# Kernel tuning notes

Hardware: AMD Instinct MI355X
Metric: run time of the kernel (lower is better)

The kernel has to match this reference:

```python
import jax, jax.numpy as jnp
import numpy as np

B, S, H = 4, 2048, 2048          # batch, seq_len, hidden_size
NH, NKV, D = 8, 1, 256           # query heads, kv heads (MQA), head_dim
ROPE_THETA = 10000.0
SCALE = D ** -0.5


def setup_inputs() -> dict:
    key = jax.random.key(0)
    k1, k2, k3 = jax.random.split(key, 3)
    hidden_states = jax.random.normal(k1, (B, S, H), dtype=jnp.float32)
    w_qkv = jax.random.normal(k2, (H, (NH + 2 * NKV) * D), dtype=jnp.float32) * 0.02
    w_o = jax.random.normal(k3, (NH * D, H), dtype=jnp.float32) * 0.02
    positions = jnp.arange(S, dtype=jnp.int32)
    return {"hidden_states": hidden_states, "positions": positions,
            "w_qkv": w_qkv, "w_o": w_o}


def _apply_rope(x, positions):
    # x: [B, S, n_heads, D], neox style: rotate halves
    d2 = D // 2
    inv_freq = 1.0 / (ROPE_THETA ** (jnp.arange(0, d2, dtype=jnp.float32) * 2.0 / D))
    ang = positions.astype(jnp.float32)[:, None] * inv_freq[None, :]      # [S, d2]
    cos = jnp.cos(ang)[None, :, None, :]                                  # [1,S,1,d2]
    sin = jnp.sin(ang)[None, :, None, :]
    x1, x2 = x[..., :d2], x[..., d2:]
    return jnp.concatenate([x1 * cos - x2 * sin, x2 * cos + x1 * sin], axis=-1)


def reference(hidden_states, positions, w_qkv, w_o):
    # fused QKV projection
    qkv = jnp.einsum('bsh,hd->bsd', hidden_states, w_qkv)                 # [B,S,(NH+2NKV)*D]
    q_size, kv_size = NH * D, NKV * D
    q = qkv[..., :q_size].reshape(B, S, NH, D)
    k = qkv[..., q_size:q_size + kv_size].reshape(B, S, NKV, D)
    v = qkv[..., q_size + kv_size:].reshape(B, S, NKV, D)

    q = _apply_rope(q, positions)
    k = _apply_rope(k, positions)

    # expand KV heads for MQA/GQA
    rep = NH // NKV
    k = jnp.repeat(k, rep, axis=2)                                        # [B,S,NH,D]
    v = jnp.repeat(v, rep, axis=2)

    scores = jnp.einsum('bqhd,bkhd->bhqk', q, k) * SCALE                  # [B,NH,S,S]
    causal = jnp.tril(jnp.ones((S, S), dtype=bool))
    scores = jnp.where(causal[None, None], scores, jnp.finfo(scores.dtype).min)
    probs = jax.nn.softmax(scores, axis=-1)
    attn = jnp.einsum('bhqk,bkhd->bqhd', probs, v).reshape(B, S, NH * D)

    return jnp.einsum('bsd,dh->bsh', attn, w_o)                           # [B,S,H]
```

## Files before the change

kernel.cpp:

```cpp
#include <hip/hip_runtime.h>
#include <math.h>

constexpr int BATCH = 4;
constexpr int SEQ   = 2048;
constexpr int HID   = 2048;
constexpr int NHEAD = 8;
constexpr int HD    = 256;
constexpr int QKVN  = (NHEAD + 2) * HD;
constexpr float SCL = 0.0625f;

typedef __bf16 bf16_t;
typedef __bf16 bf16x8 __attribute__((ext_vector_type(8)));
typedef float  f32x4  __attribute__((ext_vector_type(4)));

__device__ __forceinline__ f32x4 zero4() {
  f32x4 z; z[0] = 0.f; z[1] = 0.f; z[2] = 0.f; z[3] = 0.f; return z;
}

__device__ __forceinline__ f32x4 mfma16(bf16x8 a, bf16x8 b, f32x4 c) {
  return __builtin_amdgcn_mfma_f32_16x16x32_bf16(a, b, c, 0, 0, 0);
}

__device__ __forceinline__ void gl2lds16(const void* g, void* lds) {
  typedef __attribute__((address_space(1))) void* gp_t;
  typedef __attribute__((address_space(3))) void* lp_t;
  __builtin_amdgcn_global_load_lds((gp_t)(size_t)g,
                                   (lp_t)(unsigned int)(size_t)lds, 16, 0, 0);
}

__device__ __forceinline__ float rmax16(float v) {
#pragma unroll
  for (int o = 1; o < 16; o <<= 1) v = fmaxf(v, __shfl_xor(v, o));
  return v;
}
__device__ __forceinline__ float rsum16(float v) {
#pragma unroll
  for (int o = 1; o < 16; o <<= 1) v += __shfl_xor(v, o);
  return v;
}

__global__ __launch_bounds__(256)
void cvt_bf16_kernel(const float* __restrict__ in, bf16_t* __restrict__ out) {
  const int i = blockIdx.x * 256 + threadIdx.x;
  const float4 a = ((const float4*)in)[i * 2];
  const float4 b = ((const float4*)in)[i * 2 + 1];
  bf16x8 o;
  o[0] = (bf16_t)a.x; o[1] = (bf16_t)a.y; o[2] = (bf16_t)a.z; o[3] = (bf16_t)a.w;
  o[4] = (bf16_t)b.x; o[5] = (bf16_t)b.y; o[6] = (bf16_t)b.z; o[7] = (bf16_t)b.w;
  ((bf16x8*)out)[i] = o;
}

__global__ __launch_bounds__(256)
void transw_kernel(const float* __restrict__ w, bf16_t* __restrict__ wT, int K, int N) {
  __shared__ __align__(16) bf16_t tile[64][72];
  const int n0 = blockIdx.x * 64, k0 = blockIdx.y * 64;
  const int t = threadIdx.x, rr = t >> 3, c8 = (t & 7) * 8;
#pragma unroll
  for (int it = 0; it < 2; ++it) {
    const int r = rr + it * 32;
    const float4* p = (const float4*)(w + (size_t)(k0 + r) * N + n0 + c8);
    const float4 a = p[0], b = p[1];
    bf16x8 o;
    o[0] = (bf16_t)a.x; o[1] = (bf16_t)a.y; o[2] = (bf16_t)a.z; o[3] = (bf16_t)a.w;
    o[4] = (bf16_t)b.x; o[5] = (bf16_t)b.y; o[6] = (bf16_t)b.z; o[7] = (bf16_t)b.w;
    *(bf16x8*)&tile[r][c8] = o;
  }
  __syncthreads();
#pragma unroll
  for (int it = 0; it < 2; ++it) {
    const int rn = rr + it * 32;
    bf16x8 o;
#pragma unroll
    for (int j = 0; j < 8; ++j) o[j] = tile[c8 + j][rn];
    *(bf16x8*)&wT[(size_t)(n0 + rn) * K + k0 + c8] = o;
  }
}

#define BAR()   __builtin_amdgcn_s_barrier()
#define LGKM0() do { asm volatile("s_waitcnt lgkmcnt(0)" ::: "memory"); \
                     __builtin_amdgcn_sched_barrier(0); } while (0)
#define VMC(n)  asm volatile("s_waitcnt vmcnt(" #n ")" ::: "memory")

template <typename TC>
__global__ __launch_bounds__(512)
void gemm256_kernel(const bf16_t* __restrict__ A, const bf16_t* __restrict__ BT,
                    TC* __restrict__ C, int M, int N, int K) {
  __shared__ __align__(16) bf16_t As[2][2][128 * 64];
  __shared__ __align__(16) bf16_t Bs[2][2][128 * 64];

  const int tid = threadIdx.x;
  const int w = tid >> 6, lane = tid & 63;
  const int wr = w >> 2, wc = w & 3;
  const int quad = lane >> 4, l15 = lane & 15;
  const int bm = blockIdx.y * 256, bn = blockIdx.x * 256;

  const int srow = tid >> 3;
  const int sc16 = (tid & 7) ^ (srow & 7);
  const bf16_t* Asrc = A  + (size_t)(bm + srow) * K + sc16 * 8;
  const bf16_t* Bsrc = BT + (size_t)(bn + srow) * K + sc16 * 8;

#define STAGE_A(t, h) do {                                                  \
    const bf16_t* _s = Asrc + (size_t)((h) * 128) * K + (t) * 64;           \
    gl2lds16(_s,                 &As[(t) & 1][h][w * 512]);                 \
    gl2lds16(_s + (size_t)64 * K, &As[(t) & 1][h][4096 + w * 512]);         \
  } while (0)
#define STAGE_B(t, h) do {                                                  \
    const bf16_t* _s = Bsrc + (size_t)((h) * 128) * K + (t) * 64;           \
    gl2lds16(_s,                 &Bs[(t) & 1][h][w * 512]);                 \
    gl2lds16(_s + (size_t)64 * K, &Bs[(t) & 1][h][4096 + w * 512]);         \
  } while (0)

  const int c0  = ((quad ^ (l15 & 7)) << 3);
  const int aro = l15 * 64;
  const int bh  = wc >> 1;
  const int bro = ((wc & 1) * 64 + l15) * 64;

  f32x4 acc[8][4];
#pragma unroll
  for (int mt = 0; mt < 8; ++mt)
#pragma unroll
    for (int nt = 0; nt < 4; ++nt) acc[mt][nt] = zero4();

  bf16x8 bfr[4][2], a01[2][2], a2[6][2];

#define LD_B(b) do { _Pragma("unroll")                                      \
    for (int nt = 0; nt < 4; ++nt) {                                        \
      bfr[nt][0] = *(const bf16x8*)&Bs[b][bh][bro + nt * 1024 + c0];        \
      bfr[nt][1] = *(const bf16x8*)&Bs[b][bh][bro + nt * 1024 + (c0 ^ 32)]; \
    } } while (0)
#define LD_A01(b) do { _Pragma("unroll")                                    \
    for (int mt = 0; mt < 2; ++mt) {                                        \
      a01[mt][0] = *(const bf16x8*)&As[b][wr][aro + mt * 1024 + c0];        \
      a01[mt][1] = *(const bf16x8*)&As[b][wr][aro + mt * 1024 + (c0 ^ 32)]; \
    } } while (0)
#define LD_A2(b) do { _Pragma("unroll")                                     \
    for (int i = 0; i < 6; ++i) {                                           \
      a2[i][0] = *(const bf16x8*)&As[b][wr][aro + (i + 2) * 1024 + c0];     \
      a2[i][1] = *(const bf16x8*)&As[b][wr][aro + (i + 2) * 1024 + (c0^32)];\
    } } while (0)
#define MFMA8(A0, A1, mb) do {                                              \
    __builtin_amdgcn_s_setprio(1);                                          \
    _Pragma("unroll")                                                       \
    for (int nt = 0; nt < 4; ++nt) {                                        \
      acc[(mb)][nt]     = mfma16((A0)[0], bfr[nt][0], acc[(mb)][nt]);       \
      acc[(mb)][nt]     = mfma16((A0)[1], bfr[nt][1], acc[(mb)][nt]);       \
      acc[(mb)+1][nt]   = mfma16((A1)[0], bfr[nt][0], acc[(mb)+1][nt]);     \
      acc[(mb)+1][nt]   = mfma16((A1)[1], bfr[nt][1], acc[(mb)+1][nt]);     \
    }                                                                       \
    __builtin_amdgcn_s_setprio(0);                                          \
  } while (0)

  const int NITER = K >> 7;

  STAGE_A(0, 0); STAGE_A(0, 1); STAGE_B(0, 0); STAGE_B(0, 1);
  STAGE_A(1, 0); STAGE_A(1, 1);
  VMC(4);
  BAR();

  for (int u = 0; u < NITER; ++u) {
    const bool last = (u == NITER - 1);
    const int t1 = 2 * u + 1, t2 = 2 * u + 2, t3 = 2 * u + 3;

    LD_B(0); LD_A01(0);
    STAGE_B(t1, 0);
    BAR(); LGKM0();
    MFMA8(a01[0], a01[1], 0);
    BAR();
    LD_A2(0);
    STAGE_B(t1, 1);
    BAR(); LGKM0();
    MFMA8(a2[0], a2[1], 2);
    BAR();
    if (!last) STAGE_A(t2, 0);
    BAR();
    MFMA8(a2[2], a2[3], 4);
    BAR();
    if (!last) { STAGE_A(t2, 1); VMC(4); } else { VMC(0); }
    BAR();
    MFMA8(a2[4], a2[5], 6);
    BAR();
    LD_B(1); LD_A01(1);
    if (!last) STAGE_B(t2, 0);
    BAR(); LGKM0();
    MFMA8(a01[0], a01[1], 0);
    BAR();
    LD_A2(1);
    if (!last) STAGE_B(t2, 1);
    BAR(); LGKM0();
    MFMA8(a2[0], a2[1], 2);
    BAR();
    if (!last) STAGE_A(t3, 0);
    BAR();
    MFMA8(a2[2], a2[3], 4);
    BAR();
    if (!last) { STAGE_A(t3, 1); VMC(4); }
    BAR();
    MFMA8(a2[4], a2[5], 6);
    BAR();
  }

#pragma unroll
  for (int mt = 0; mt < 8; ++mt)
#pragma unroll
    for (int nt = 0; nt < 4; ++nt)
#pragma unroll
      for (int r = 0; r < 4; ++r) {
        const int row = bm + wr * 128 + mt * 16 + quad * 4 + r;
        const int col = bn + wc * 64 + nt * 16 + l15;
        C[(size_t)row * N + col] = (TC)acc[mt][nt][r];
      }
#undef STAGE_A
#undef STAGE_B
#undef LD_B
#undef LD_A01
#undef LD_A2
#undef MFMA8
}

__global__ __launch_bounds__(128)
void rope_table_kernel(const int* __restrict__ pos, float2* __restrict__ tab) {
  const int s = blockIdx.x, i = threadIdx.x;
  const float inv_freq = powf(10000.0f, -(float)i / 128.0f);
  const float ang = (float)pos[s] * inv_freq;
  float sn, cs;
  sincosf(ang, &sn, &cs);
  tab[s * 128 + i] = make_float2(cs, sn);
}

__global__ __launch_bounds__(256)
void rope_kernel(const float2* __restrict__ tab, bf16_t* __restrict__ qkv) {
  const int bs = blockIdx.x * 16 + (threadIdx.x >> 4);
  const int h  = blockIdx.y;
  const int i0 = (threadIdx.x & 15) * 8;
  const int s  = bs & (SEQ - 1);
  const size_t base = (size_t)bs * QKVN + (size_t)h * HD;
  bf16x8 a = *(const bf16x8*)&qkv[base + i0];
  bf16x8 b = *(const bf16x8*)&qkv[base + 128 + i0];
  bf16x8 oa, ob;
#pragma unroll
  for (int j = 0; j < 8; ++j) {
    const float2 t = tab[s * 128 + i0 + j];
    const float x1 = (float)a[j], x2 = (float)b[j];
    oa[j] = (bf16_t)(x1 * t.x - x2 * t.y);
    ob[j] = (bf16_t)(x2 * t.x + x1 * t.y);
  }
  *(bf16x8*)&qkv[base + i0]       = oa;
  *(bf16x8*)&qkv[base + 128 + i0] = ob;
}

__global__ __launch_bounds__(256)
void vtrans_kernel(const bf16_t* __restrict__ qkv, bf16_t* __restrict__ Vt) {
  __shared__ __align__(16) bf16_t tile[64][72];
  const int s0 = blockIdx.x * 64, d0 = blockIdx.y * 64, b = blockIdx.z;
  const int t = threadIdx.x, rr = t >> 3, c8 = (t & 7) * 8;
#pragma unroll
  for (int it = 0; it < 2; ++it) {
    const int r = rr + it * 32;
    *(bf16x8*)&tile[r][c8] =
        *(const bf16x8*)&qkv[(size_t)(b * SEQ + s0 + r) * QKVN + 2304 + d0 + c8];
  }
  __syncthreads();
#pragma unroll
  for (int it = 0; it < 2; ++it) {
    const int dd = rr + it * 32;
    bf16x8 o;
#pragma unroll
    for (int j = 0; j < 8; ++j) o[j] = tile[c8 + j][dd];
    *(bf16x8*)&Vt[(size_t)(b * HD + d0 + dd) * SEQ + s0 + c8] = o;
  }
}

__global__ __launch_bounds__(512)
void attn_kernel(const bf16_t* __restrict__ qkv, const bf16_t* __restrict__ Vt,
                 bf16_t* __restrict__ O) {
  __shared__ __align__(16) bf16_t Ks[64 * 256];
  __shared__ __align__(16) bf16_t Vts[256 * 64];

  const int tid = threadIdx.x, w = tid >> 6, lane = tid & 63;
  const int quad = lane >> 4, l15 = lane & 15;
  const int bid = blockIdx.x;
  const int qtR = bid & 63;
  const int b = (bid >> 6) & 3;
  const int qt = (bid >> 8) ? (127 - qtR) : qtR;
  const int h = w;
  const int q0 = qt * 16;

  bf16_t* PKs = &Ks[w * 1024];

  const int krow_base = w * 2 + (lane >> 5);
  const int kcol = lane & 31;
  const int vrow_base = w * 8 + (lane >> 3);
  const int vcol = lane & 7;

  const bf16_t* kbase0 = qkv + (size_t)(b * SEQ) * QKVN + 2048;
  const bf16_t* vbase0 = Vt + (size_t)b * HD * SEQ;

  bf16x8 qf[8];
  const bf16_t* qp =
      qkv + (size_t)(b * SEQ + q0 + l15) * QKVN + (size_t)h * HD + quad * 8;
#pragma unroll
  for (int ks = 0; ks < 8; ++ks) qf[ks] = *(const bf16x8*)(qp + ks * 32);

  float mrun[4], lrun[4];
  f32x4 of[16];
#pragma unroll
  for (int r = 0; r < 4; ++r) { mrun[r] = -3e38f; lrun[r] = 0.f; }
#pragma unroll
  for (int dt = 0; dt < 16; ++dt) of[dt] = zero4();

  const int ntiles = q0 / 64 + 1;

  for (int kt = 0; kt < ntiles; ++kt) {
    const bf16_t* kbase = kbase0 + (size_t)(kt * 64) * QKVN;
#pragma unroll
    for (int i = 0; i < 4; ++i) {
      const int r = i * 16 + krow_base;
      gl2lds16(kbase + (size_t)r * QKVN + ((kcol ^ (r & 31)) << 3),
               &Ks[(i * 512 + w * 64) * 8]);
    }
    const bf16_t* vbase = vbase0 + kt * 64;
#pragma unroll
    for (int i = 0; i < 4; ++i) {
      const int r = i * 64 + vrow_base;
      gl2lds16(vbase + (size_t)r * SEQ + ((vcol ^ (r & 7)) << 3),
               &Vts[(i * 512 + w * 64) * 8]);
    }
    __syncthreads();

    f32x4 sf[4];
#pragma unroll
    for (int nt = 0; nt < 4; ++nt) {
      f32x4 acc = zero4();
      const int row = nt * 16 + l15;
#pragma unroll
      for (int ks = 0; ks < 8; ++ks) {
        const int jj = ks * 4 + quad;
        const bf16x8 kf = *(const bf16x8*)&Ks[row * 256 + ((jj ^ (row & 31)) << 3)];
        acc = mfma16(qf[ks], kf, acc);
      }
      sf[nt] = acc;
    }

    const bool lastTile = (kt == ntiles - 1);
    float mx[4];
#pragma unroll
    for (int r = 0; r < 4; ++r) {
      const int qg = q0 + quad * 4 + r;
      float v = -3e38f;
#pragma unroll
      for (int nt = 0; nt < 4; ++nt) {
        float s = sf[nt][r] * SCL;
        if (lastTile) {
          const int kg = kt * 64 + nt * 16 + l15;
          if (kg > qg) s = -3e38f;
        }
        sf[nt][r] = s;
        v = fmaxf(v, s);
      }
      mx[r] = rmax16(v);
    }

    float g = 0.f;
#pragma unroll
    for (int r = 0; r < 4; ++r) g = fmaxf(g, mx[r] - mrun[r]);
    const bool resc = !__all(g <= 8.0f);
    f32x4 av;
    if (resc) {
#pragma unroll
      for (int r = 0; r < 4; ++r) {
        const float mn = fmaxf(mrun[r], mx[r]);
        av[r] = __expf(mrun[r] - mn);
        mrun[r] = mn;
        lrun[r] *= av[r];
      }
    }

    __syncthreads();

#pragma unroll
    for (int r = 0; r < 4; ++r) {
      const int rowp = quad * 4 + r;
      float sum = 0.f;
#pragma unroll
      for (int nt = 0; nt < 4; ++nt) {
        const float pv = __expf(sf[nt][r] - mrun[r]);
        PKs[rowp * 64 + ((((nt * 2 + (l15 >> 3)) ^ (rowp & 7)) << 3) + (l15 & 7))] =
            (bf16_t)pv;
        sum += pv;
      }
      lrun[r] += rsum16(sum);
    }
    if (resc) {
#pragma unroll
      for (int dt = 0; dt < 16; ++dt) of[dt] *= av;
    }
    __asm__ volatile("s_waitcnt lgkmcnt(0)" ::: "memory");

    bf16x8 pa[2];
#pragma unroll
    for (int k2 = 0; k2 < 2; ++k2)
      pa[k2] = *(const bf16x8*)&PKs[l15 * 64 + (((k2 * 4 + quad) ^ (l15 & 7)) << 3)];
#pragma unroll
    for (int dt = 0; dt < 16; ++dt) {
      const int row = dt * 16 + l15;
#pragma unroll
      for (int k2 = 0; k2 < 2; ++k2) {
        const int jj = k2 * 4 + quad;
        const bf16x8 vf = *(const bf16x8*)&Vts[row * 64 + ((jj ^ (row & 7)) << 3)];
        of[dt] = mfma16(pa[k2], vf, of[dt]);
      }
    }

    __syncthreads();
  }

  f32x4 iv;
#pragma unroll
  for (int r = 0; r < 4; ++r) iv[r] = 1.0f / lrun[r];
#pragma unroll
  for (int dt = 0; dt < 16; ++dt) {
    const f32x4 o = of[dt] * iv;
#pragma unroll
    for (int r = 0; r < 4; ++r)
      O[(size_t)(b * SEQ + q0 + quad * 4 + r) * HID + (size_t)h * HD + dt * 16 + l15] =
          (bf16_t)o[r];
  }
}

extern "C" void kernel_launch(void* const* d_in, const int* in_sizes, int n_in,
                              void* d_out, int out_size, void* d_ws, size_t ws_size,
                              hipStream_t stream) {
  const float* hidden  = (const float*)d_in[0];
  const int* positions = (const int*)d_in[1];
  const float* w_qkv   = (const float*)d_in[2];
  const float* w_o     = (const float*)d_in[3];
  float* out           = (float*)d_out;

  char* ws = (char*)d_ws;
  bf16_t* hiddenB = (bf16_t*)ws; ws += (size_t)8192 * 2048 * 2;
  bf16_t* wqkvT   = (bf16_t*)ws; ws += (size_t)2560 * 2048 * 2;
  bf16_t* woT     = (bf16_t*)ws; ws += (size_t)2048 * 2048 * 2;
  bf16_t* qkvB    = (bf16_t*)ws; ws += (size_t)8192 * 2560 * 2;
  bf16_t* VtB     = (bf16_t*)ws; ws += (size_t)4 * 256 * 2048 * 2;
  bf16_t* attnB   = (bf16_t*)ws;

  float2* ropeTab = (float2*)attnB;

  cvt_bf16_kernel<<<8192, 256, 0, stream>>>(hidden, hiddenB);
  transw_kernel<<<dim3(QKVN / 64, HID / 64), 256, 0, stream>>>(w_qkv, wqkvT, HID, QKVN);
  transw_kernel<<<dim3(HID / 64, HID / 64), 256, 0, stream>>>(w_o, woT, HID, HID);
  rope_table_kernel<<<SEQ, 128, 0, stream>>>(positions, ropeTab);

  gemm256_kernel<bf16_t><<<dim3(QKVN / 256, 8192 / 256), 512, 0, stream>>>
      (hiddenB, wqkvT, qkvB, 8192, QKVN, HID);

  rope_kernel<<<dim3(BATCH * SEQ / 16, 9), 256, 0, stream>>>(ropeTab, qkvB);
  vtrans_kernel<<<dim3(SEQ / 64, HD / 64, BATCH), 256, 0, stream>>>(qkvB, VtB);

  attn_kernel<<<512, 512, 0, stream>>>(qkvB, VtB, attnB);

  gemm256_kernel<float><<<dim3(HID / 256, 8192 / 256), 512, 0, stream>>>
      (attnB, woT, out, 8192, HID, HID);
}
```

Measured before the change: 518.0 us.

## Double attention block to 16 waves sharing K/V tiles across two query tiles

The attention kernel now launches 256 blocks of 1024 threads. Each block has 16 waves: 8 heads times 2 adjacent 16-row query tiles, so every K/V tile loaded into LDS serves twice as many queries. Each block handles a pair of query-tile groups, one from the front of the sequence and a mirrored one from the back, to balance causal work across blocks. This halves global K/V traffic per query and the number of loads issued per thread. In exchange, the register budget per thread is tighter under 1024-thread launch bounds, there are fewer blocks to fill the GPU, and the extra waves add barrier contention.

```diff
diff --git a/kernel.cpp b/kernel.cpp
--- a/kernel.cpp
+++ b/kernel.cpp
@@ -270,7 +270,7 @@
   }
 }
 
-__global__ __launch_bounds__(512)
+__global__ __launch_bounds__(1024)
 void attn_kernel(const bf16_t* __restrict__ qkv, const bf16_t* __restrict__ Vt,
                  bf16_t* __restrict__ O) {
   __shared__ __align__(16) bf16_t Ks[64 * 256];
@@ -278,152 +278,148 @@
 
   const int tid = threadIdx.x, w = tid >> 6, lane = tid & 63;
   const int quad = lane >> 4, l15 = lane & 15;
-  const int bid = blockIdx.x;
-  const int qtR = bid & 63;
-  const int b = (bid >> 6) & 3;
-  const int qt = (bid >> 8) ? (127 - qtR) : qtR;
-  const int h = w;
-  const int q0 = qt * 16;
+  const int b = blockIdx.x >> 6;
+  const int j = blockIdx.x & 63;
+  const int h = w & 7;
+  const int g = w >> 3;
 
   bf16_t* PKs = &Ks[w * 1024];
-
-  const int krow_base = w * 2 + (lane >> 5);
-  const int kcol = lane & 31;
-  const int vrow_base = w * 8 + (lane >> 3);
-  const int vcol = lane & 7;
 
   const bf16_t* kbase0 = qkv + (size_t)(b * SEQ) * QKVN + 2048;
   const bf16_t* vbase0 = Vt + (size_t)b * HD * SEQ;
 
-  bf16x8 qf[8];
-  const bf16_t* qp =
-      qkv + (size_t)(b * SEQ + q0 + l15) * QKVN + (size_t)h * HD + quad * 8;
-#pragma unroll
-  for (int ks = 0; ks < 8; ++ks) qf[ks] = *(const bf16x8*)(qp + ks * 32);
-
-  float mrun[4], lrun[4];
-  f32x4 of[16];
-#pragma unroll
-  for (int r = 0; r < 4; ++r) { mrun[r] = -3e38f; lrun[r] = 0.f; }
-#pragma unroll
-  for (int dt = 0; dt < 16; ++dt) of[dt] = zero4();
-
-  const int ntiles = q0 / 64 + 1;
-
-  for (int kt = 0; kt < ntiles; ++kt) {
-    const bf16_t* kbase = kbase0 + (size_t)(kt * 64) * QKVN;
-#pragma unroll
-    for (int i = 0; i < 4; ++i) {
-      const int r = i * 16 + krow_base;
-      gl2lds16(kbase + (size_t)r * QKVN + ((kcol ^ (r & 31)) << 3),
-               &Ks[(i * 512 + w * 64) * 8]);
+  for (int p = 0; p < 2; ++p) {
+    const int base = p ? (126 - 2 * j) : (2 * j);
+    const int qt = base + g;
+    const int q0 = qt * 16;
+    const int ntiles = base / 4 + 1;
+
+    bf16x8 qf[8];
+    const bf16_t* qp =
+        qkv + (size_t)(b * SEQ + q0 + l15) * QKVN + (size_t)h * HD + quad * 8;
+#pragma unroll
+    for (int ks = 0; ks < 8; ++ks) qf[ks] = *(const bf16x8*)(qp + ks * 32);
+
+    float mrun[4], lrun[4];
+    f32x4 of[16];
+#pragma unroll
+    for (int r = 0; r < 4; ++r) { mrun[r] = -3e38f; lrun[r] = 0.f; }
+#pragma unroll
+    for (int dt = 0; dt < 16; ++dt) of[dt] = zero4();
+
+    for (int kt = 0; kt < ntiles; ++kt) {
+      const bf16_t* kbase = kbase0 + (size_t)(kt * 64) * QKVN;
+      const bf16_t* vbase = vbase0 + kt * 64;
+#pragma unroll
+      for (int i = 0; i < 2; ++i) {
+        const int c = i * 1024 + tid;
+        const int kr = c >> 5, kc = c & 31;
+        gl2lds16(kbase + (size_t)kr * QKVN + ((kc ^ (kr & 31)) << 3),
+                 &Ks[(i * 1024 + w * 64) * 8]);
+        const int vr = c >> 3, vc = c & 7;
+        gl2lds16(vbase + (size_t)vr * SEQ + ((vc ^ (vr & 7)) << 3),
+                 &Vts[(i * 1024 + w * 64) * 8]);
+      }
+      __syncthreads();
+
+      f32x4 sf[4];
+#pragma unroll
+      for (int nt = 0; nt < 4; ++nt) {
+        f32x4 acc = zero4();
+        const int row = nt * 16 + l15;
+#pragma unroll
+        for (int ks = 0; ks < 8; ++ks) {
+          const int jj = ks * 4 + quad;
+          const bf16x8 kf = *(const bf16x8*)&Ks[row * 256 + ((jj ^ (row & 31)) << 3)];
+          acc = mfma16(qf[ks], kf, acc);
+        }
+        sf[nt] = acc;
+      }
+
+      const bool lastTile = (kt == ntiles - 1);
+      float mx[4];
+#pragma unroll
+      for (int r = 0; r < 4; ++r) {
+        const int qg = q0 + quad * 4 + r;
+        float v = -3e38f;
+#pragma unroll
+        for (int nt = 0; nt < 4; ++nt) {
+          float s = sf[nt][r] * SCL;
+          if (lastTile) {
+            const int kg = kt * 64 + nt * 16 + l15;
+            if (kg > qg) s = -3e38f;
+          }
+          sf[nt][r] = s;
+          v = fmaxf(v, s);
+        }
+        mx[r] = rmax16(v);
+      }
+
+      float gg = 0.f;
+#pragma unroll
+      for (int r = 0; r < 4; ++r) gg = fmaxf(gg, mx[r] - mrun[r]);
+      const bool resc = !__all(gg <= 8.0f);
+      f32x4 av;
+      if (resc) {
+#pragma unroll
+        for (int r = 0; r < 4; ++r) {
+          const float mn = fmaxf(mrun[r], mx[r]);
+          av[r] = __expf(mrun[r] - mn);
+          mrun[r] = mn;
+          lrun[r] *= av[r];
+        }
+      }
+
+      __syncthreads();
+
+#pragma unroll
+      for (int r = 0; r < 4; ++r) {
+        const int rowp = quad * 4 + r;
+        float sum = 0.f;
+#pragma unroll
+        for (int nt = 0; nt < 4; ++nt) {
+          const float pv = __expf(sf[nt][r] - mrun[r]);
+          PKs[rowp * 64 + ((((nt * 2 + (l15 >> 3)) ^ (rowp & 7)) << 3) + (l15 & 7))] =
+              (bf16_t)pv;
+          sum += pv;
+        }
+        lrun[r] += rsum16(sum);
+      }
+      if (resc) {
+#pragma unroll
+        for (int dt = 0; dt < 16; ++dt) of[dt] *= av;
+      }
+      __asm__ volatile("s_waitcnt lgkmcnt(0)" ::: "memory");
+
+      bf16x8 pa[2];
+#pragma unroll
+      for (int k2 = 0; k2 < 2; ++k2)
+        pa[k2] = *(const bf16x8*)&PKs[l15 * 64 + (((k2 * 4 + quad) ^ (l15 & 7)) << 3)];
+#pragma unroll
+      for (int dt = 0; dt < 16; ++dt) {
+        const int row = dt * 16 + l15;
+#pragma unroll
+        for (int k2 = 0; k2 < 2; ++k2) {
+          const int jj = k2 * 4 + quad;
+          const bf16x8 vf = *(const bf16x8*)&Vts[row * 64 + ((jj ^ (row & 7)) << 3)];
+          of[dt] = mfma16(pa[k2], vf, of[dt]);
+        }
+      }
+
+      __syncthreads();
     }
-    const bf16_t* vbase = vbase0 + kt * 64;
-#pragma unroll
-    for (int i = 0; i < 4; ++i) {
-      const int r = i * 64 + vrow_base;
-      gl2lds16(vbase + (size_t)r * SEQ + ((vcol ^ (r & 7)) << 3),
-               &Vts[(i * 512 + w * 64) * 8]);
+
+    f32x4 iv;
+#pragma unroll
+    for (int r = 0; r < 4; ++r) iv[r] = 1.0f / lrun[r];
+#pragma unroll
+    for (int dt = 0; dt < 16; ++dt) {
+      const f32x4 o = of[dt] * iv;
+#pragma unroll
+      for (int r = 0; r < 4; ++r)
+        O[(size_t)(b * SEQ + q0 + quad * 4 + r) * HID + (size_t)h * HD + dt * 16 + l15] =
+            (bf16_t)o[r];
     }
-    __syncthreads();
-
-    f32x4 sf[4];
-#pragma unroll
-    for (int nt = 0; nt < 4; ++nt) {
-      f32x4 acc = zero4();
-      const int row = nt * 16 + l15;
-#pragma unroll
-      for (int ks = 0; ks < 8; ++ks) {
-        const int jj = ks * 4 + quad;
-        const bf16x8 kf = *(const bf16x8*)&Ks[row * 256 + ((jj ^ (row & 31)) << 3)];
-        acc = mfma16(qf[ks], kf, acc);
-      }
-      sf[nt] = acc;
-    }
-
-    const bool lastTile = (kt == ntiles - 1);
-    float mx[4];
-#pragma unroll
-    for (int r = 0; r < 4; ++r) {
-      const int qg = q0 + quad * 4 + r;
-      float v = -3e38f;
-#pragma unroll
-      for (int nt = 0; nt < 4; ++nt) {
-        float s = sf[nt][r] * SCL;
-        if (lastTile) {
-          const int kg = kt * 64 + nt * 16 + l15;
-          if (kg > qg) s = -3e38f;
-        }
-        sf[nt][r] = s;
-        v = fmaxf(v, s);
-      }
-      mx[r] = rmax16(v);
-    }
-
-    float g = 0.f;
-#pragma unroll
-    for (int r = 0; r < 4; ++r) g = fmaxf(g, mx[r] - mrun[r]);
-    const bool resc = !__all(g <= 8.0f);
-    f32x4 av;
-    if (resc) {
-#pragma unroll
-      for (int r = 0; r < 4; ++r) {
-        const float mn = fmaxf(mrun[r], mx[r]);
-        av[r] = __expf(mrun[r] - mn);
-        mrun[r] = mn;
-        lrun[r] *= av[r];
-      }
-    }
-
-    __syncthreads();
-
-#pragma unroll
-    for (int r = 0; r < 4; ++r) {
-      const int rowp = quad * 4 + r;
-      float sum = 0.f;
-#pragma unroll
-      for (int nt = 0; nt < 4; ++nt) {
-        const float pv = __expf(sf[nt][r] - mrun[r]);
-        PKs[rowp * 64 + ((((nt * 2 + (l15 >> 3)) ^ (rowp & 7)) << 3) + (l15 & 7))] =
-            (bf16_t)pv;
-        sum += pv;
-      }
-      lrun[r] += rsum16(sum);
-    }
-    if (resc) {
-#pragma unroll
-      for (int dt = 0; dt < 16; ++dt) of[dt] *= av;
-    }
-    __asm__ volatile("s_waitcnt lgkmcnt(0)" ::: "memory");
-
-    bf16x8 pa[2];
-#pragma unroll
-    for (int k2 = 0; k2 < 2; ++k2)
-      pa[k2] = *(const bf16x8*)&PKs[l15 * 64 + (((k2 * 4 + quad) ^ (l15 & 7)) << 3)];
-#pragma unroll
-    for (int dt = 0; dt < 16; ++dt) {
-      const int row = dt * 16 + l15;
-#pragma unroll
-      for (int k2 = 0; k2 < 2; ++k2) {
-        const int jj = k2 * 4 + quad;
-        const bf16x8 vf = *(const bf16x8*)&Vts[row * 64 + ((jj ^ (row & 7)) << 3)];
-        of[dt] = mfma16(pa[k2], vf, of[dt]);
-      }
-    }
-
-    __syncthreads();
-  }
-
-  f32x4 iv;
-#pragma unroll
-  for (int r = 0; r < 4; ++r) iv[r] = 1.0f / lrun[r];
-#pragma unroll
-  for (int dt = 0; dt < 16; ++dt) {
-    const f32x4 o = of[dt] * iv;
-#pragma unroll
-    for (int r = 0; r < 4; ++r)
-      O[(size_t)(b * SEQ + q0 + quad * 4 + r) * HID + (size_t)h * HD + dt * 16 + l15] =
-          (bf16_t)o[r];
   }
 }
 
@@ -457,7 +453,7 @@
   rope_kernel<<<dim3(BATCH * SEQ / 16, 9), 256, 0, stream>>>(ropeTab, qkvB);
   vtrans_kernel<<<dim3(SEQ / 64, HD / 64, BATCH), 256, 0, stream>>>(qkvB, VtB);
 
-  attn_kernel<<<512, 512, 0, stream>>>(qkvB, VtB, attnB);
+  attn_kernel<<<256, 1024, 0, stream>>>(qkvB, VtB, attnB);
 
   gemm256_kernel<float><<<dim3(HID / 256, 8192 / 256), 512, 0, stream>>>
       (attnB, woT, out, 8192, HID, HID);
```

Result: slower. 1.104 ms (+113.2%).

## Pair causal query tiles per block and widen KV tiles to 128 keys

Applied to the files above, without the earlier changes.

Each attention block now handles two query tiles, qtR and its mirror 127-qtR, one after the other, so every block does a balanced share of causal work and the grid shrinks from 512 to 256 blocks. The K and V staging tiles grow from 64 to 128 keys, which halves the number of load/sync rounds per query tile and processes two 64-key subtiles per staged tile. The cost is double the LDS (128 KB), which limits occupancy to one block per CU. With only 256 blocks, some CUs may sit idle, and the serial phases keep latency hiding low.

```diff
diff --git a/kernel.cpp b/kernel.cpp
--- a/kernel.cpp
+++ b/kernel.cpp
@@ -273,157 +273,161 @@
 __global__ __launch_bounds__(512)
 void attn_kernel(const bf16_t* __restrict__ qkv, const bf16_t* __restrict__ Vt,
                  bf16_t* __restrict__ O) {
-  __shared__ __align__(16) bf16_t Ks[64 * 256];
-  __shared__ __align__(16) bf16_t Vts[256 * 64];
+  __shared__ __align__(16) bf16_t Ks[128 * 256];
+  __shared__ __align__(16) bf16_t Vts[256 * 128];
 
   const int tid = threadIdx.x, w = tid >> 6, lane = tid & 63;
   const int quad = lane >> 4, l15 = lane & 15;
-  const int bid = blockIdx.x;
-  const int qtR = bid & 63;
-  const int b = (bid >> 6) & 3;
-  const int qt = (bid >> 8) ? (127 - qtR) : qtR;
+  const int b = blockIdx.x >> 6;
+  const int qtR = blockIdx.x & 63;
   const int h = w;
-  const int q0 = qt * 16;
 
   bf16_t* PKs = &Ks[w * 1024];
-
-  const int krow_base = w * 2 + (lane >> 5);
-  const int kcol = lane & 31;
-  const int vrow_base = w * 8 + (lane >> 3);
-  const int vcol = lane & 7;
 
   const bf16_t* kbase0 = qkv + (size_t)(b * SEQ) * QKVN + 2048;
   const bf16_t* vbase0 = Vt + (size_t)b * HD * SEQ;
 
-  bf16x8 qf[8];
-  const bf16_t* qp =
-      qkv + (size_t)(b * SEQ + q0 + l15) * QKVN + (size_t)h * HD + quad * 8;
-#pragma unroll
-  for (int ks = 0; ks < 8; ++ks) qf[ks] = *(const bf16x8*)(qp + ks * 32);
-
-  float mrun[4], lrun[4];
-  f32x4 of[16];
-#pragma unroll
-  for (int r = 0; r < 4; ++r) { mrun[r] = -3e38f; lrun[r] = 0.f; }
-#pragma unroll
-  for (int dt = 0; dt < 16; ++dt) of[dt] = zero4();
-
-  const int ntiles = q0 / 64 + 1;
-
-  for (int kt = 0; kt < ntiles; ++kt) {
-    const bf16_t* kbase = kbase0 + (size_t)(kt * 64) * QKVN;
-#pragma unroll
-    for (int i = 0; i < 4; ++i) {
-      const int r = i * 16 + krow_base;
-      gl2lds16(kbase + (size_t)r * QKVN + ((kcol ^ (r & 31)) << 3),
-               &Ks[(i * 512 + w * 64) * 8]);
+  for (int phase = 0; phase < 2; ++phase) {
+    const int qt = phase ? (127 - qtR) : qtR;
+    const int q0 = qt * 16;
+
+    bf16x8 qf[8];
+    const bf16_t* qp =
+        qkv + (size_t)(b * SEQ + q0 + l15) * QKVN + (size_t)h * HD + quad * 8;
+#pragma unroll
+    for (int ks = 0; ks < 8; ++ks) qf[ks] = *(const bf16x8*)(qp + ks * 32);
+
+    float mrun[4], lrun[4];
+    f32x4 of[16];
+#pragma unroll
+    for (int r = 0; r < 4; ++r) { mrun[r] = -3e38f; lrun[r] = 0.f; }
+#pragma unroll
+    for (int dt = 0; dt < 16; ++dt) of[dt] = zero4();
+
+    const int nt128 = q0 / 128 + 1;
+
+    for (int kt = 0; kt < nt128; ++kt) {
+      const bf16_t* kbase = kbase0 + (size_t)(kt * 128) * QKVN;
+      const bf16_t* vbase = vbase0 + kt * 128;
+#pragma unroll
+      for (int i = 0; i < 8; ++i) {
+        const int kr = i * 16 + w * 2 + (lane >> 5);
+        const int kc = lane & 31;
+        gl2lds16(kbase + (size_t)kr * QKVN + ((kc ^ (kr & 31)) << 3),
+                 &Ks[(i * 512 + w * 64) * 8]);
+        const int vr = i * 32 + w * 4 + (lane >> 4);
+        const int vc = lane & 15;
+        gl2lds16(vbase + (size_t)vr * SEQ + ((vc ^ (vr & 15)) << 3),
+                 &Vts[(i * 512 + w * 64) * 8]);
+      }
+      __syncthreads();
+
+#pragma unroll
+      for (int sub = 0; sub < 2; ++sub) {
+        const int k0g = kt * 128 + sub * 64;
+        if (k0g > q0 + 15) break;
+
+        f32x4 sf[4];
+#pragma unroll
+        for (int nt = 0; nt < 4; ++nt) {
+          f32x4 acc = zero4();
+          const int row = sub * 64 + nt * 16 + l15;
+#pragma unroll
+          for (int ks = 0; ks < 8; ++ks) {
+            const int jj = ks * 4 + quad;
+            const bf16x8 kf =
+                *(const bf16x8*)&Ks[row * 256 + ((jj ^ (row & 31)) << 3)];
+            acc = mfma16(qf[ks], kf, acc);
+          }
+          sf[nt] = acc;
+        }
+
+        const bool needMask = (k0g + 63 > q0);
+        float mx[4];
+#pragma unroll
+        for (int r = 0; r < 4; ++r) {
+          const int qg = q0 + quad * 4 + r;
+          float v = -3e38f;
+#pragma unroll
+          for (int nt = 0; nt < 4; ++nt) {
+            float s = sf[nt][r] * SCL;
+            if (needMask) {
+              const int kg = k0g + nt * 16 + l15;
+              if (kg > qg) s = -3e38f;
+            }
+            sf[nt][r] = s;
+            v = fmaxf(v, s);
+          }
+          mx[r] = rmax16(v);
+        }
+
+        float g = 0.f;
+#pragma unroll
+        for (int r = 0; r < 4; ++r) g = fmaxf(g, mx[r] - mrun[r]);
+        const bool resc = !__all(g <= 8.0f);
+        f32x4 av;
+        if (resc) {
+#pragma unroll
+          for (int r = 0; r < 4; ++r) {
+            const float mn = fmaxf(mrun[r], mx[r]);
+            av[r] = __expf(mrun[r] - mn);
+            mrun[r] = mn;
+            lrun[r] *= av[r];
+          }
+        }
+
+        if (sub == 0) __syncthreads();
+
+#pragma unroll
+        for (int r = 0; r < 4; ++r) {
+          const int rowp = quad * 4 + r;
+          float sum = 0.f;
+#pragma unroll
+          for (int nt = 0; nt < 4; ++nt) {
+            const float pv = __expf(sf[nt][r] - mrun[r]);
+            PKs[rowp * 64 + ((((nt * 2 + (l15 >> 3)) ^ (rowp & 7)) << 3) + (l15 & 7))] =
+                (bf16_t)pv;
+            sum += pv;
+          }
+          lrun[r] += rsum16(sum);
+        }
+        if (resc) {
+#pragma unroll
+          for (int dt = 0; dt < 16; ++dt) of[dt] *= av;
+        }
+        __asm__ volatile("s_waitcnt lgkmcnt(0)" ::: "memory");
+
+        bf16x8 pa[2];
+#pragma unroll
+        for (int k2 = 0; k2 < 2; ++k2)
+          pa[k2] = *(const bf16x8*)&PKs[l15 * 64 + (((k2 * 4 + quad) ^ (l15 & 7)) << 3)];
+#pragma unroll
+        for (int dt = 0; dt < 16; ++dt) {
+          const int row = dt * 16 + l15;
+#pragma unroll
+          for (int k2 = 0; k2 < 2; ++k2) {
+            const int jj = sub * 8 + k2 * 4 + quad;
+            const bf16x8 vf =
+                *(const bf16x8*)&Vts[row * 128 + ((jj ^ (row & 15)) << 3)];
+            of[dt] = mfma16(pa[k2], vf, of[dt]);
+          }
+        }
+      }
+
+      __syncthreads();
     }
-    const bf16_t* vbase = vbase0 + kt * 64;
-#pragma unroll
-    for (int i = 0; i < 4; ++i) {
-      const int r = i * 64 + vrow_base;
-      gl2lds16(vbase + (size_t)r * SEQ + ((vcol ^ (r & 7)) << 3),
-               &Vts[(i * 512 + w * 64) * 8]);
+
+    f32x4 iv;
+#pragma unroll
+    for (int r = 0; r < 4; ++r) iv[r] = 1.0f / lrun[r];
+#pragma unroll
+    for (int dt = 0; dt < 16; ++dt) {
+      const f32x4 o = of[dt] * iv;
+#pragma unroll
+      for (int r = 0; r < 4; ++r)
+        O[(size_t)(b * SEQ + q0 + quad * 4 + r) * HID + (size_t)h * HD + dt * 16 + l15] =
+            (bf16_t)o[r];
     }
-    __syncthreads();
-
-    f32x4 sf[4];
-#pragma unroll
-    for (int nt = 0; nt < 4; ++nt) {
-      f32x4 acc = zero4();
-      const int row = nt * 16 + l15;
-#pragma unroll
-      for (int ks = 0; ks < 8; ++ks) {
-        const int jj = ks * 4 + quad;
-        const bf16x8 kf = *(const bf16x8*)&Ks[row * 256 + ((jj ^ (row & 31)) << 3)];
-        acc = mfma16(qf[ks], kf, acc);
-      }
-      sf[nt] = acc;
-    }
-
-    const bool lastTile = (kt == ntiles - 1);
-    float mx[4];
-#pragma unroll
-    for (int r = 0; r < 4; ++r) {
-      const int qg = q0 + quad * 4 + r;
-      float v = -3e38f;
-#pragma unroll
-      for (int nt = 0; nt < 4; ++nt) {
-        float s = sf[nt][r] * SCL;
-        if (lastTile) {
-          const int kg = kt * 64 + nt * 16 + l15;
-          if (kg > qg) s = -3e38f;
-        }
-        sf[nt][r] = s;
-        v = fmaxf(v, s);
-      }
-      mx[r] = rmax16(v);
-    }
-
-    float g = 0.f;
-#pragma unroll
-    for (int r = 0; r < 4; ++r) g = fmaxf(g, mx[r] - mrun[r]);
-    const bool resc = !__all(g <= 8.0f);
-    f32x4 av;
-    if (resc) {
-#pragma unroll
-      for (int r = 0; r < 4; ++r) {
-        const float mn = fmaxf(mrun[r], mx[r]);
-        av[r] = __expf(mrun[r] - mn);
-        mrun[r] = mn;
-        lrun[r] *= av[r];
-      }
-    }
-
-    __syncthreads();
-
-#pragma unroll
-    for (int r = 0; r < 4; ++r) {
-      const int rowp = quad * 4 + r;
-      float sum = 0.f;
-#pragma unroll
-      for (int nt = 0; nt < 4; ++nt) {
-        const float pv = __expf(sf[nt][r] - mrun[r]);
-        PKs[rowp * 64 + ((((nt * 2 + (l15 >> 3)) ^ (rowp & 7)) << 3) + (l15 & 7))] =
-            (bf16_t)pv;
-        sum += pv;
-      }
-      lrun[r] += rsum16(sum);
-    }
-    if (resc) {
-#pragma unroll
-      for (int dt = 0; dt < 16; ++dt) of[dt] *= av;
-    }
-    __asm__ volatile("s_waitcnt lgkmcnt(0)" ::: "memory");
-
-    bf16x8 pa[2];
-#pragma unroll
-    for (int k2 = 0; k2 < 2; ++k2)
-      pa[k2] = *(const bf16x8*)&PKs[l15 * 64 + (((k2 * 4 + quad) ^ (l15 & 7)) << 3)];
-#pragma unroll
-    for (int dt = 0; dt < 16; ++dt) {
-      const int row = dt * 16 + l15;
-#pragma unroll
-      for (int k2 = 0; k2 < 2; ++k2) {
-        const int jj = k2 * 4 + quad;
-        const bf16x8 vf = *(const bf16x8*)&Vts[row * 64 + ((jj ^ (row & 7)) << 3)];
-        of[dt] = mfma16(pa[k2], vf, of[dt]);
-      }
-    }
-
-    __syncthreads();
-  }
-
-  f32x4 iv;
-#pragma unroll
-  for (int r = 0; r < 4; ++r) iv[r] = 1.0f / lrun[r];
-#pragma unroll
-  for (int dt = 0; dt < 16; ++dt) {
-    const f32x4 o = of[dt] * iv;
-#pragma unroll
-    for (int r = 0; r < 4; ++r)
-      O[(size_t)(b * SEQ + q0 + quad * 4 + r) * HID + (size_t)h * HD + dt * 16 + l15] =
-          (bf16_t)o[r];
   }
 }
 
@@ -457,7 +461,7 @@
   rope_kernel<<<dim3(BATCH * SEQ / 16, 9), 256, 0, stream>>>(ropeTab, qkvB);
   vtrans_kernel<<<dim3(SEQ / 64, HD / 64, BATCH), 256, 0, stream>>>(qkvB, VtB);
 
-  attn_kernel<<<512, 512, 0, stream>>>(qkvB, VtB, attnB);
+  attn_kernel<<<256, 512, 0, stream>>>(qkvB, VtB, attnB);
 
   gemm256_kernel<float><<<dim3(HID / 256, 8192 / 256), 512, 0, stream>>>
       (attnB, woT, out, 8192, HID, HID);
```

Result: faster. 483.7 us (-6.6%).
